# Performance work log

Measured on AMD Instinct MI355X. Metric: run time of the kernel, lower is better.

Reference implementation:

```python
import jax, jax.numpy as jnp
import numpy as np

N, E, B = 50000, 800000, 512
DIN, H, G, M = 128, 128, 32, 128
EPS = 1e-5


def _gcn_layer(h, src, dst, W, b):
    h = h @ W  # [N, H]
    loop = jnp.arange(N)
    s = jnp.concatenate([src, loop])
    d = jnp.concatenate([dst, loop])
    deg = jax.ops.segment_sum(jnp.ones(s.shape, h.dtype), d, num_segments=N)
    dinv = jax.lax.rsqrt(jnp.maximum(deg, 1.0))  # deg >= 1 due to self-loops
    norm = dinv[s] * dinv[d]  # [E+N]
    out = jax.ops.segment_sum(norm[:, None] * h[s], d, num_segments=N)
    return out + b


def _bn_relu(h, gamma, beta):
    mu = jnp.mean(h, axis=0)
    var = jnp.mean((h - mu) ** 2, axis=0)
    return jax.nn.relu((h - mu) * jax.lax.rsqrt(var + EPS) * gamma + beta)


def setup_inputs() -> dict:
    key = jax.random.key(0)
    ks = jax.random.split(key, 20)
    inp = {
        "x": jax.random.normal(ks[0], (N, DIN), jnp.float32),
        "edge_index": jax.random.randint(ks[1], (2, E), 0, N),
        "batch": jnp.sort(jax.random.randint(ks[2], (N,), 0, B)),
        "global_feats": jax.random.normal(ks[3], (B, G), jnp.float32),
    }
    dims = [DIN, H, H]
    for i in range(3):
        inp[f"W{i}"] = jax.random.normal(ks[4 + i], (dims[i], H), jnp.float32) / np.sqrt(dims[i])
        inp[f"b{i}"] = jnp.zeros((H,), jnp.float32)
        inp[f"g{i}"] = jnp.ones((H,), jnp.float32)
        inp[f"be{i}"] = jnp.zeros((H,), jnp.float32)
    inp["M1w"] = jax.random.normal(ks[10], (H + G, M), jnp.float32) / np.sqrt(H + G)
    inp["M1b"] = jnp.zeros((M,), jnp.float32)
    inp["M2w"] = jax.random.normal(ks[11], (M, M // 2), jnp.float32) / np.sqrt(M)
    inp["M2b"] = jnp.zeros((M // 2,), jnp.float32)
    inp["M3w"] = jax.random.normal(ks[12], (M // 2, 1), jnp.float32) / np.sqrt(M // 2)
    inp["M3b"] = jnp.zeros((1,), jnp.float32)
    return inp


def reference(x, edge_index, batch, global_feats,
              W0, b0, g0, be0, W1, b1, g1, be1, W2, b2, g2, be2,
              M1w, M1b, M2w, M2b, M3w, M3b):
    src, dst = edge_index[0], edge_index[1]
    h = x
    for W, b, g, be in ((W0, b0, g0, be0), (W1, b1, g1, be1), (W2, b2, g2, be2)):
        h = _bn_relu(_gcn_layer(h, src, dst, W, b), g, be)
    # global mean pool over graphs
    sums = jax.ops.segment_sum(h, batch, num_segments=B)  # [B, H]
    cnt = jax.ops.segment_sum(jnp.ones((N,), h.dtype), batch, num_segments=B)
    pooled = sums / jnp.maximum(cnt, 1.0)[:, None]
    z = jnp.concatenate([pooled, global_feats], axis=1)  # [B, H+G]
    z = jax.nn.relu(z @ M1w + M1b)
    z = jax.nn.relu(z @ M2w + M2b)
    out = z @ M3w + M3b  # [B, 1]
    return out.reshape(-1)
```

## Files before the change

kernel.cpp:

```cpp
#include <hip/hip_runtime.h>

#define NN 50000
#define NE 800000
#define BG 512
#define HD 128
#define GD 32
#define MD 128
#define EPSV 1e-5f
#define NBK 256
#define BSTR 196
#define BCAP 4096
#define SP 136
#define CSB 128

typedef __attribute__((ext_vector_type(8))) short bf16x8;
typedef __attribute__((ext_vector_type(4))) float f32x4;

static __device__ __forceinline__ unsigned short f2bf(float f) {
    unsigned int u = __float_as_uint(f);
    u += 0x7fffu + ((u >> 16) & 1u);
    return (unsigned short)(u >> 16);
}
static __device__ __forceinline__ float bfu(unsigned short v) {
    return __uint_as_float((unsigned int)v << 16);
}
static __device__ __forceinline__ float bf_lo(unsigned int v) {
    return __uint_as_float(v << 16);
}
static __device__ __forceinline__ float bf_hi(unsigned int v) {
    return __uint_as_float(v & 0xffff0000u);
}

__global__ __launch_bounds__(256) void k_bin(const int* __restrict__ src,
                                             const int* __restrict__ dst,
                                             int* __restrict__ bucket_cnt,
                                             unsigned int* __restrict__ binned) {
    __shared__ int hcnt[NBK];
    __shared__ int hbase[NBK];
    int tid = threadIdx.x;
    int e0 = blockIdx.x * 2048;
    unsigned int pv[8];
    int bk[8], rk[8];
#pragma unroll
    for (int i = 0; i < 8; ++i) {
        int e = e0 + i * 256 + tid;
        if (e < NE) {
            int s = src[e];
            int d = dst[e];
            bk[i] = d / BSTR;
            pv[i] = ((unsigned int)(d - bk[i] * BSTR) << 16) | (unsigned int)s;
        } else {
            bk[i] = -1;
        }
    }
    hcnt[tid] = 0;
    __syncthreads();
#pragma unroll
    for (int i = 0; i < 8; ++i)
        if (bk[i] >= 0) rk[i] = atomicAdd(&hcnt[bk[i]], 1);
    __syncthreads();
    hbase[tid] = atomicAdd(&bucket_cnt[tid], hcnt[tid]);
    __syncthreads();
#pragma unroll
    for (int i = 0; i < 8; ++i)
        if (bk[i] >= 0)
            binned[(size_t)bk[i] * BCAP + hbase[bk[i]] + rk[i]] = pv[i];
}

__global__ __launch_bounds__(256) void k_csr(const unsigned int* __restrict__ binned,
                                             const int* __restrict__ bucket_cnt,
                                             int* __restrict__ offsets,
                                             float* __restrict__ dinv,
                                             int* __restrict__ csr,
                                             const float* __restrict__ W0,
                                             const float* __restrict__ W1,
                                             const float* __restrict__ W2,
                                             unsigned short* __restrict__ Wt) {
    __shared__ unsigned short sW[128 * 130];
    __shared__ int ls[256];
    __shared__ int h[BSTR];
    __shared__ int cur[BSTR];
    __shared__ int bpre_s;
    int b = blockIdx.x, t = threadIdx.x;
    if (b >= NBK) {
        const float* Wsrc = (b == NBK) ? W0 : ((b == NBK + 1) ? W1 : W2);
#pragma unroll
        for (int i = 0; i < 64; ++i) {
            int idx = i * 256 + t;
            int k = idx >> 7, n = idx & 127;
            sW[n * 130 + k] = f2bf(Wsrc[idx]);
        }
        __syncthreads();
        unsigned short* o = Wt + (size_t)(b - NBK) * 16384;
#pragma unroll
        for (int i = 0; i < 64; ++i) {
            int idx = i * 256 + t;
            int n = idx >> 7, k = idx & 127;
            o[idx] = sW[n * 130 + k];
        }
        return;
    }
    int bc = bucket_cnt[t];
    ls[t] = bc;
    __syncthreads();
    for (int off = 1; off < 256; off <<= 1) {
        int c0 = ls[t];
        int add = (t >= off) ? ls[t - off] : 0;
        __syncthreads();
        ls[t] = c0 + add;
        __syncthreads();
    }
    if (t == b) bpre_s = ls[t] - bc;
    if (t < BSTR) h[t] = 0;
    __syncthreads();
    int bpre = bpre_s;
    int nb = bucket_cnt[b];
    const unsigned int* base = binned + (size_t)b * BCAP;
    for (int e = t; e < nb; e += 256)
        atomicAdd(&h[base[e] >> 16], 1);
    __syncthreads();
    int c = (t < BSTR) ? h[t] : 0;
    ls[t] = c;
    __syncthreads();
    for (int off = 1; off < 256; off <<= 1) {
        int c0 = ls[t];
        int add = (t >= off) ? ls[t - off] : 0;
        __syncthreads();
        ls[t] = c0 + add;
        __syncthreads();
    }
    int node = b * BSTR + t;
    if (t < BSTR) {
        int excl = ls[t] - c + bpre;
        cur[t] = excl;
        if (node < NN) {
            offsets[node] = excl;
            dinv[node] = rsqrtf((float)(c + 1));
            if (node == NN - 1) offsets[NN] = NE;
        }
    }
    __syncthreads();
    for (int e = t; e < nb; e += 256) {
        unsigned int v = base[e];
        int pos = atomicAdd(&cur[v >> 16], 1);
        csr[pos] = (int)(v & 0xffffu);
    }
}

__global__ __launch_bounds__(256) void k_gemm(const float* __restrict__ Inf,
                                              const unsigned short* __restrict__ Inh,
                                              const unsigned short* __restrict__ Wt,
                                              unsigned short* __restrict__ Th,
                                              const float* __restrict__ stats,
                                              const float* __restrict__ gamma,
                                              const float* __restrict__ beta,
                                              const float* __restrict__ dinv,
                                              int useBN) {
    __shared__ unsigned short Abf[64 * SP];
    __shared__ unsigned short WtL[128 * SP];
    __shared__ float ssS[256];
    int tid = threadIdx.x;
    int rowBase = blockIdx.x * 64;
    if (useBN) {
        ssS[tid] = stats[tid];
        __syncthreads();
        if (tid < 128) {
            float mu = ssS[tid] * (1.f / NN);
            float var = ssS[128 + tid] * (1.f / NN) - mu * mu;
            float sc = gamma[tid] * rsqrtf(var + EPSV);
            float sh = beta[tid] - mu * sc;
            ssS[tid] = sc;
            ssS[128 + tid] = sh;
        }
        __syncthreads();
#pragma unroll
        for (int i = 0; i < 4; ++i) {
            int q = tid + i * 256;
            int row = q >> 4;
            int k8 = (q & 15) * 8;
            int rg = rowBase + row;
            if (rg >= NN) rg = NN - 1;
            bf16x8 raw = *(const bf16x8*)&Inh[(size_t)rg * HD + k8];
            unsigned short o[8];
#pragma unroll
            for (int e = 0; e < 8; ++e) {
                float v = bfu((unsigned short)raw[e]);
                v = fmaxf(v * ssS[k8 + e] + ssS[128 + k8 + e], 0.f);
                o[e] = f2bf(v);
            }
            *(bf16x8*)&Abf[row * SP + k8] = *(bf16x8*)o;
        }
    } else {
#pragma unroll
        for (int i = 0; i < 8; ++i) {
            int q = tid + i * 256;
            int row = q >> 5;
            int c4 = (q & 31) * 4;
            int rg = rowBase + row;
            if (rg >= NN) rg = NN - 1;
            float4 v = *(const float4*)&Inf[(size_t)rg * HD + c4];
            unsigned short* p = &Abf[row * SP + c4];
            p[0] = f2bf(v.x); p[1] = f2bf(v.y); p[2] = f2bf(v.z); p[3] = f2bf(v.w);
        }
    }
#pragma unroll
    for (int i = 0; i < 8; ++i) {
        int q = tid + i * 256;
        int n = q >> 4;
        int k8 = (q & 15) * 8;
        bf16x8 w = *(const bf16x8*)&Wt[n * HD + k8];
        *(bf16x8*)&WtL[n * SP + k8] = w;
    }
    __syncthreads();
    int lane = tid & 63;
    int wv = tid >> 6;
    int quad = lane >> 4;
    int lrow = wv * 16 + (lane & 15);
    f32x4 acc[8];
#pragma unroll
    for (int c = 0; c < 8; ++c) acc[c] = (f32x4){0.f, 0.f, 0.f, 0.f};
#pragma unroll
    for (int qk = 0; qk < 4; ++qk) {
        int ko = quad * 8 + qk * 32;
        bf16x8 bfr = *(const bf16x8*)&Abf[lrow * SP + ko];
#pragma unroll
        for (int c = 0; c < 8; ++c) {
            bf16x8 afr = *(const bf16x8*)&WtL[(c * 16 + (lane & 15)) * SP + ko];
            acc[c] = __builtin_amdgcn_mfma_f32_16x16x32_bf16(afr, bfr, acc[c], 0, 0, 0);
        }
    }
    int grow = rowBase + lrow;
    if (grow < NN) {
        float di = dinv[grow];
#pragma unroll
        for (int c = 0; c < 8; ++c) {
            ushort4 o;
            o.x = f2bf(acc[c][0] * di);
            o.y = f2bf(acc[c][1] * di);
            o.z = f2bf(acc[c][2] * di);
            o.w = f2bf(acc[c][3] * di);
            *(ushort4*)&Th[(size_t)grow * HD + c * 16 + quad * 4] = o;
        }
    }
}

__global__ __launch_bounds__(256, 8) void k_aggregate(const uint4* __restrict__ T4,
                                                      const int* __restrict__ offsets,
                                                      const int* __restrict__ csr,
                                                      const float* __restrict__ dinv,
                                                      const float* __restrict__ bias,
                                                      unsigned short* __restrict__ Ah) {
    int d = blockIdx.x * 4 + (threadIdx.x >> 6);
    int l = threadIdx.x & 63;
    int half = l >> 4;
    int li = l & 15;
    if (d >= NN) return;
    int start = offsets[d], end = offsets[d + 1];
    float a0 = 0.f, a1 = 0.f, a2 = 0.f, a3 = 0.f;
    float a4 = 0.f, a5 = 0.f, a6 = 0.f, a7 = 0.f;
    int j = start;
    for (; j + 7 < end; j += 8) {
        int s0 = csr[j + half];
        int s1 = csr[j + 4 + half];
        uint4 v0 = T4[(size_t)s0 * 16 + li];
        uint4 v1 = T4[(size_t)s1 * 16 + li];
        a0 += bf_lo(v0.x); a1 += bf_hi(v0.x); a2 += bf_lo(v0.y); a3 += bf_hi(v0.y);
        a4 += bf_lo(v0.z); a5 += bf_hi(v0.z); a6 += bf_lo(v0.w); a7 += bf_hi(v0.w);
        a0 += bf_lo(v1.x); a1 += bf_hi(v1.x); a2 += bf_lo(v1.y); a3 += bf_hi(v1.y);
        a4 += bf_lo(v1.z); a5 += bf_hi(v1.z); a6 += bf_lo(v1.w); a7 += bf_hi(v1.w);
    }
    for (; j + 3 < end; j += 4) {
        int s0 = csr[j + half];
        uint4 v0 = T4[(size_t)s0 * 16 + li];
        a0 += bf_lo(v0.x); a1 += bf_hi(v0.x); a2 += bf_lo(v0.y); a3 += bf_hi(v0.y);
        a4 += bf_lo(v0.z); a5 += bf_hi(v0.z); a6 += bf_lo(v0.w); a7 += bf_hi(v0.w);
    }
    if (j + half < end) {
        int s0 = csr[j + half];
        uint4 v0 = T4[(size_t)s0 * 16 + li];
        a0 += bf_lo(v0.x); a1 += bf_hi(v0.x); a2 += bf_lo(v0.y); a3 += bf_hi(v0.y);
        a4 += bf_lo(v0.z); a5 += bf_hi(v0.z); a6 += bf_lo(v0.w); a7 += bf_hi(v0.w);
    }
    a0 += __shfl_xor(a0, 16); a1 += __shfl_xor(a1, 16);
    a2 += __shfl_xor(a2, 16); a3 += __shfl_xor(a3, 16);
    a4 += __shfl_xor(a4, 16); a5 += __shfl_xor(a5, 16);
    a6 += __shfl_xor(a6, 16); a7 += __shfl_xor(a7, 16);
    a0 += __shfl_xor(a0, 32); a1 += __shfl_xor(a1, 32);
    a2 += __shfl_xor(a2, 32); a3 += __shfl_xor(a3, 32);
    a4 += __shfl_xor(a4, 32); a5 += __shfl_xor(a5, 32);
    a6 += __shfl_xor(a6, 32); a7 += __shfl_xor(a7, 32);
    if (half == 0) {
        float di = dinv[d];
        uint4 vd = T4[(size_t)d * 16 + li];
        float4 bs0 = *(const float4*)&bias[8 * li];
        float4 bs1 = *(const float4*)&bias[8 * li + 4];
        unsigned short o[8];
        o[0] = f2bf(di * (a0 + bf_lo(vd.x)) + bs0.x);
        o[1] = f2bf(di * (a1 + bf_hi(vd.x)) + bs0.y);
        o[2] = f2bf(di * (a2 + bf_lo(vd.y)) + bs0.z);
        o[3] = f2bf(di * (a3 + bf_hi(vd.y)) + bs0.w);
        o[4] = f2bf(di * (a4 + bf_lo(vd.z)) + bs1.x);
        o[5] = f2bf(di * (a5 + bf_hi(vd.z)) + bs1.y);
        o[6] = f2bf(di * (a6 + bf_lo(vd.w)) + bs1.z);
        o[7] = f2bf(di * (a7 + bf_hi(vd.w)) + bs1.w);
        *(bf16x8*)&Ah[(size_t)d * HD + 8 * li] = *(bf16x8*)o;
    }
}

__global__ __launch_bounds__(256) void k_colstats(const uint2* __restrict__ A2,
                                                  float* __restrict__ stats) {
    int li = threadIdx.x & 31;
    int rr = threadIdx.x >> 5;
    float4 s = {0.f, 0.f, 0.f, 0.f}, q = {0.f, 0.f, 0.f, 0.f};
    for (int row = blockIdx.x * 8 + rr; row < NN; row += CSB * 8) {
        uint2 u = A2[(size_t)row * 32 + li];
        float x0 = bf_lo(u.x), x1 = bf_hi(u.x), x2 = bf_lo(u.y), x3 = bf_hi(u.y);
        s.x += x0; s.y += x1; s.z += x2; s.w += x3;
        q.x += x0 * x0; q.y += x1 * x1; q.z += x2 * x2; q.w += x3 * x3;
    }
    __shared__ float4 lsum[256], lqum[256];
    lsum[threadIdx.x] = s;
    lqum[threadIdx.x] = q;
    __syncthreads();
    if (rr == 0) {
        float4 a = lsum[li];
#pragma unroll
        for (int g = 1; g < 8; ++g) {
            float4 b = lsum[g * 32 + li];
            a.x += b.x; a.y += b.y; a.z += b.z; a.w += b.w;
        }
        atomicAdd(&stats[4 * li + 0], a.x);
        atomicAdd(&stats[4 * li + 1], a.y);
        atomicAdd(&stats[4 * li + 2], a.z);
        atomicAdd(&stats[4 * li + 3], a.w);
    } else if (rr == 1) {
        float4 a = lqum[li];
#pragma unroll
        for (int g = 1; g < 8; ++g) {
            float4 b = lqum[g * 32 + li];
            a.x += b.x; a.y += b.y; a.z += b.z; a.w += b.w;
        }
        atomicAdd(&stats[128 + 4 * li + 0], a.x);
        atomicAdd(&stats[128 + 4 * li + 1], a.y);
        atomicAdd(&stats[128 + 4 * li + 2], a.z);
        atomicAdd(&stats[128 + 4 * li + 3], a.w);
    }
}

__global__ __launch_bounds__(256) void k_pool(const unsigned int* __restrict__ Au,
                                              const int* __restrict__ batch,
                                              const float* __restrict__ stats,
                                              const float* __restrict__ gamma,
                                              const float* __restrict__ beta,
                                              float* __restrict__ pooled) {
    __shared__ float ssP[256];
    int t = threadIdx.x;
    ssP[t] = stats[t];
    __syncthreads();
    if (t < 128) {
        float mu = ssP[t] * (1.f / NN);
        float var = ssP[128 + t] * (1.f / NN) - mu * mu;
        float sc = gamma[t] * rsqrtf(var + EPSV);
        float sh = beta[t] - mu * sc;
        ssP[t] = sc;
        ssP[128 + t] = sh;
    }
    __syncthreads();
    int fu = t & 63;
    int half = t >> 6;
    int r0 = blockIdx.x * 64;
    int rend = min(r0 + 64, NN);
    float s0 = ssP[2 * fu], s1 = ssP[2 * fu + 1];
    float h0 = ssP[128 + 2 * fu], h1 = ssP[128 + 2 * fu + 1];
    float a0 = 0.f, a1 = 0.f;
    int cg = -1;
    for (int r = r0 + half; r < rend; r += 4) {
        int g = batch[r];
        if (g != cg) {
            if (cg >= 0) {
                atomicAdd(&pooled[(size_t)cg * HD + 2 * fu], a0);
                atomicAdd(&pooled[(size_t)cg * HD + 2 * fu + 1], a1);
            }
            cg = g;
            a0 = 0.f; a1 = 0.f;
        }
        unsigned int v = Au[(size_t)r * 64 + fu];
        a0 += fmaxf(bf_lo(v) * s0 + h0, 0.f);
        a1 += fmaxf(bf_hi(v) * s1 + h1, 0.f);
    }
    if (cg >= 0) {
        atomicAdd(&pooled[(size_t)cg * HD + 2 * fu], a0);
        atomicAdd(&pooled[(size_t)cg * HD + 2 * fu + 1], a1);
    }
}

__global__ __launch_bounds__(128) void k_mlp(const float* __restrict__ pooled,
                                             const int* __restrict__ batch,
                                             const float* __restrict__ gfeat,
                                             const float* __restrict__ M1w,
                                             const float* __restrict__ M1b,
                                             const float* __restrict__ M2w,
                                             const float* __restrict__ M2b,
                                             const float* __restrict__ M3w,
                                             const float* __restrict__ M3b,
                                             float* __restrict__ out) {
    __shared__ int sb[2];
    __shared__ float z[HD + GD];
    __shared__ float z1[MD];
    __shared__ float z2[MD / 2];
    int b = blockIdx.x, t = threadIdx.x;
    if (t < 2) {
        int val = b + t;
        int lo = 0, hi = NN;
        while (lo < hi) {
            int mid = (lo + hi) >> 1;
            if (batch[mid] < val) lo = mid + 1; else hi = mid;
        }
        sb[t] = lo;
    }
    __syncthreads();
    float ic = 1.f / fmaxf((float)(sb[1] - sb[0]), 1.f);
    z[t] = pooled[(size_t)b * HD + t] * ic;
    if (t < GD) z[HD + t] = gfeat[b * GD + t];
    __syncthreads();
    float a = M1b[t];
    for (int k = 0; k < HD + GD; ++k) a += z[k] * M1w[k * MD + t];
    z1[t] = fmaxf(a, 0.f);
    __syncthreads();
    if (t < MD / 2) {
        float a2 = M2b[t];
        for (int k = 0; k < MD; ++k) a2 += z1[k] * M2w[k * (MD / 2) + t];
        z2[t] = fmaxf(a2, 0.f);
    }
    __syncthreads();
    if (t < 64) {
        float p = z2[t] * M3w[t];
#pragma unroll
        for (int off = 32; off; off >>= 1) p += __shfl_down(p, off);
        if (t == 0) out[b] = p + M3b[0];
    }
}

static inline size_t alg(size_t x) { return (x + 255) & ~(size_t)255; }

extern "C" void kernel_launch(void* const* d_in, const int* in_sizes, int n_in,
                              void* d_out, int out_size, void* d_ws, size_t ws_size,
                              hipStream_t stream) {
    const float* x = (const float*)d_in[0];
    const int* ei = (const int*)d_in[1];
    const int* batch = (const int*)d_in[2];
    const float* gf = (const float*)d_in[3];
    const float* W[3] = {(const float*)d_in[4], (const float*)d_in[8], (const float*)d_in[12]};
    const float* bb[3] = {(const float*)d_in[5], (const float*)d_in[9], (const float*)d_in[13]};
    const float* gg[3] = {(const float*)d_in[6], (const float*)d_in[10], (const float*)d_in[14]};
    const float* be[3] = {(const float*)d_in[7], (const float*)d_in[11], (const float*)d_in[15]};
    const float* M1w = (const float*)d_in[16];
    const float* M1b = (const float*)d_in[17];
    const float* M2w = (const float*)d_in[18];
    const float* M2b = (const float*)d_in[19];
    const float* M3w = (const float*)d_in[20];
    const float* M3b = (const float*)d_in[21];
    float* out = (float*)d_out;

    char* w = (char*)d_ws;
    int* bucket_cnt = (int*)w;    w += alg((size_t)NBK * 4);
    float* pooled = (float*)w;    w += alg((size_t)BG * HD * 4);
    float* stats = (float*)w;     w += alg((size_t)3 * 256 * 4);
    size_t zspan = (size_t)(w - (char*)d_ws);
    int* offsets = (int*)w;       w += alg((size_t)(NN + 1) * 4);
    int* csr = (int*)w;           w += alg((size_t)NE * 4);
    float* dinv = (float*)w;      w += alg((size_t)NN * 4);
    unsigned short* Wt = (unsigned short*)w;  w += alg((size_t)3 * 16384 * 2);
    unsigned int* binned = (unsigned int*)w;  w += alg((size_t)NBK * BCAP * 4);
    unsigned short* Ah = (unsigned short*)w;  w += alg((size_t)NN * HD * 2);
    unsigned short* Th = (unsigned short*)w;  w += alg((size_t)NN * HD * 2);

    const int* src = ei;
    const int* dst = ei + NE;

    hipMemsetAsync(bucket_cnt, 0, zspan, stream);
    k_bin<<<(NE + 2047) / 2048, 256, 0, stream>>>(src, dst, bucket_cnt, binned);
    k_csr<<<NBK + 3, 256, 0, stream>>>(binned, bucket_cnt, offsets, dinv, csr,
                                       W[0], W[1], W[2], Wt);

    for (int L = 0; L < 3; ++L) {
        k_gemm<<<(NN + 63) / 64, 256, 0, stream>>>(x, Ah, Wt + (size_t)L * 16384, Th,
                                                   stats + (L ? (L - 1) * 256 : 0),
                                                   gg[L ? L - 1 : 0], be[L ? L - 1 : 0],
                                                   dinv, L > 0);
        k_aggregate<<<(NN + 3) / 4, 256, 0, stream>>>((const uint4*)Th, offsets, csr,
                                                      dinv, bb[L], Ah);
        k_colstats<<<CSB, 256, 0, stream>>>((const uint2*)Ah, stats + L * 256);
    }

    k_pool<<<(NN + 63) / 64, 256, 0, stream>>>((const unsigned int*)Ah, batch,
                                               stats + 2 * 256, gg[2], be[2], pooled);
    k_mlp<<<BG, 128, 0, stream>>>(pooled, batch, gf, M1w, M1b, M2w, M2b, M3w, M3b, out);
}
```

Measured before the change: 368.4 us.

## Fuse BN column stats into aggregate and pooling into MLP kernel

Column sum and sum-of-squares statistics are now gathered inside k_aggregate through shared-memory atomics, then written to 64 partial slots in global memory that k_gemm and k_mlp add up. This removes the separate k_colstats pass that reread Ah after each layer. k_pool is also dropped: k_mlp now applies BN+ReLU and mean-pools each graph's contiguous node range directly. In exchange every aggregate block does 16 LDS atomics per node and a global atomic per thread, and each MLP block reduces 64 partial slots.

```diff
diff --git a/kernel.cpp b/kernel.cpp
--- a/kernel.cpp
+++ b/kernel.cpp
@@ -11,7 +11,7 @@
 #define BSTR 196
 #define BCAP 4096
 #define SP 136
-#define CSB 128
+#define NSC 64
 
 typedef __attribute__((ext_vector_type(8))) short bf16x8;
 typedef __attribute__((ext_vector_type(4))) float f32x4;
@@ -151,7 +151,7 @@
                                               const unsigned short* __restrict__ Inh,
                                               const unsigned short* __restrict__ Wt,
                                               unsigned short* __restrict__ Th,
-                                              const float* __restrict__ stats,
+                                              const float* __restrict__ statsP,
                                               const float* __restrict__ gamma,
                                               const float* __restrict__ beta,
                                               const float* __restrict__ dinv,
@@ -162,7 +162,9 @@
     int tid = threadIdx.x;
     int rowBase = blockIdx.x * 64;
     if (useBN) {
-        ssS[tid] = stats[tid];
+        float s = 0.f;
+        for (int c = 0; c < NSC; ++c) s += statsP[c * 256 + tid];
+        ssS[tid] = s;
         __syncthreads();
         if (tid < 128) {
             float mu = ssS[tid] * (1.f / NN);
@@ -249,153 +251,88 @@
                                                       const int* __restrict__ csr,
                                                       const float* __restrict__ dinv,
                                                       const float* __restrict__ bias,
-                                                      unsigned short* __restrict__ Ah) {
-    int d = blockIdx.x * 4 + (threadIdx.x >> 6);
-    int l = threadIdx.x & 63;
+                                                      unsigned short* __restrict__ Ah,
+                                                      float* __restrict__ statsP) {
+    __shared__ float sst[256];
+    int tid = threadIdx.x;
+    sst[tid] = 0.f;
+    __syncthreads();
+    int d = blockIdx.x * 4 + (tid >> 6);
+    int l = tid & 63;
     int half = l >> 4;
     int li = l & 15;
-    if (d >= NN) return;
-    int start = offsets[d], end = offsets[d + 1];
-    float a0 = 0.f, a1 = 0.f, a2 = 0.f, a3 = 0.f;
-    float a4 = 0.f, a5 = 0.f, a6 = 0.f, a7 = 0.f;
-    int j = start;
-    for (; j + 7 < end; j += 8) {
-        int s0 = csr[j + half];
-        int s1 = csr[j + 4 + half];
-        uint4 v0 = T4[(size_t)s0 * 16 + li];
-        uint4 v1 = T4[(size_t)s1 * 16 + li];
-        a0 += bf_lo(v0.x); a1 += bf_hi(v0.x); a2 += bf_lo(v0.y); a3 += bf_hi(v0.y);
-        a4 += bf_lo(v0.z); a5 += bf_hi(v0.z); a6 += bf_lo(v0.w); a7 += bf_hi(v0.w);
-        a0 += bf_lo(v1.x); a1 += bf_hi(v1.x); a2 += bf_lo(v1.y); a3 += bf_hi(v1.y);
-        a4 += bf_lo(v1.z); a5 += bf_hi(v1.z); a6 += bf_lo(v1.w); a7 += bf_hi(v1.w);
-    }
-    for (; j + 3 < end; j += 4) {
-        int s0 = csr[j + half];
-        uint4 v0 = T4[(size_t)s0 * 16 + li];
-        a0 += bf_lo(v0.x); a1 += bf_hi(v0.x); a2 += bf_lo(v0.y); a3 += bf_hi(v0.y);
-        a4 += bf_lo(v0.z); a5 += bf_hi(v0.z); a6 += bf_lo(v0.w); a7 += bf_hi(v0.w);
-    }
-    if (j + half < end) {
-        int s0 = csr[j + half];
-        uint4 v0 = T4[(size_t)s0 * 16 + li];
-        a0 += bf_lo(v0.x); a1 += bf_hi(v0.x); a2 += bf_lo(v0.y); a3 += bf_hi(v0.y);
-        a4 += bf_lo(v0.z); a5 += bf_hi(v0.z); a6 += bf_lo(v0.w); a7 += bf_hi(v0.w);
-    }
-    a0 += __shfl_xor(a0, 16); a1 += __shfl_xor(a1, 16);
-    a2 += __shfl_xor(a2, 16); a3 += __shfl_xor(a3, 16);
-    a4 += __shfl_xor(a4, 16); a5 += __shfl_xor(a5, 16);
-    a6 += __shfl_xor(a6, 16); a7 += __shfl_xor(a7, 16);
-    a0 += __shfl_xor(a0, 32); a1 += __shfl_xor(a1, 32);
-    a2 += __shfl_xor(a2, 32); a3 += __shfl_xor(a3, 32);
-    a4 += __shfl_xor(a4, 32); a5 += __shfl_xor(a5, 32);
-    a6 += __shfl_xor(a6, 32); a7 += __shfl_xor(a7, 32);
-    if (half == 0) {
-        float di = dinv[d];
-        uint4 vd = T4[(size_t)d * 16 + li];
-        float4 bs0 = *(const float4*)&bias[8 * li];
-        float4 bs1 = *(const float4*)&bias[8 * li + 4];
-        unsigned short o[8];
-        o[0] = f2bf(di * (a0 + bf_lo(vd.x)) + bs0.x);
-        o[1] = f2bf(di * (a1 + bf_hi(vd.x)) + bs0.y);
-        o[2] = f2bf(di * (a2 + bf_lo(vd.y)) + bs0.z);
-        o[3] = f2bf(di * (a3 + bf_hi(vd.y)) + bs0.w);
-        o[4] = f2bf(di * (a4 + bf_lo(vd.z)) + bs1.x);
-        o[5] = f2bf(di * (a5 + bf_hi(vd.z)) + bs1.y);
-        o[6] = f2bf(di * (a6 + bf_lo(vd.w)) + bs1.z);
-        o[7] = f2bf(di * (a7 + bf_hi(vd.w)) + bs1.w);
-        *(bf16x8*)&Ah[(size_t)d * HD + 8 * li] = *(bf16x8*)o;
-    }
-}
-
-__global__ __launch_bounds__(256) void k_colstats(const uint2* __restrict__ A2,
-                                                  float* __restrict__ stats) {
-    int li = threadIdx.x & 31;
-    int rr = threadIdx.x >> 5;
-    float4 s = {0.f, 0.f, 0.f, 0.f}, q = {0.f, 0.f, 0.f, 0.f};
-    for (int row = blockIdx.x * 8 + rr; row < NN; row += CSB * 8) {
-        uint2 u = A2[(size_t)row * 32 + li];
-        float x0 = bf_lo(u.x), x1 = bf_hi(u.x), x2 = bf_lo(u.y), x3 = bf_hi(u.y);
-        s.x += x0; s.y += x1; s.z += x2; s.w += x3;
-        q.x += x0 * x0; q.y += x1 * x1; q.z += x2 * x2; q.w += x3 * x3;
-    }
-    __shared__ float4 lsum[256], lqum[256];
-    lsum[threadIdx.x] = s;
-    lqum[threadIdx.x] = q;
-    __syncthreads();
-    if (rr == 0) {
-        float4 a = lsum[li];
-#pragma unroll
-        for (int g = 1; g < 8; ++g) {
-            float4 b = lsum[g * 32 + li];
-            a.x += b.x; a.y += b.y; a.z += b.z; a.w += b.w;
-        }
-        atomicAdd(&stats[4 * li + 0], a.x);
-        atomicAdd(&stats[4 * li + 1], a.y);
-        atomicAdd(&stats[4 * li + 2], a.z);
-        atomicAdd(&stats[4 * li + 3], a.w);
-    } else if (rr == 1) {
-        float4 a = lqum[li];
-#pragma unroll
-        for (int g = 1; g < 8; ++g) {
-            float4 b = lqum[g * 32 + li];
-            a.x += b.x; a.y += b.y; a.z += b.z; a.w += b.w;
-        }
-        atomicAdd(&stats[128 + 4 * li + 0], a.x);
-        atomicAdd(&stats[128 + 4 * li + 1], a.y);
-        atomicAdd(&stats[128 + 4 * li + 2], a.z);
-        atomicAdd(&stats[128 + 4 * li + 3], a.w);
-    }
-}
-
-__global__ __launch_bounds__(256) void k_pool(const unsigned int* __restrict__ Au,
-                                              const int* __restrict__ batch,
-                                              const float* __restrict__ stats,
-                                              const float* __restrict__ gamma,
-                                              const float* __restrict__ beta,
-                                              float* __restrict__ pooled) {
-    __shared__ float ssP[256];
-    int t = threadIdx.x;
-    ssP[t] = stats[t];
-    __syncthreads();
-    if (t < 128) {
-        float mu = ssP[t] * (1.f / NN);
-        float var = ssP[128 + t] * (1.f / NN) - mu * mu;
-        float sc = gamma[t] * rsqrtf(var + EPSV);
-        float sh = beta[t] - mu * sc;
-        ssP[t] = sc;
-        ssP[128 + t] = sh;
-    }
-    __syncthreads();
-    int fu = t & 63;
-    int half = t >> 6;
-    int r0 = blockIdx.x * 64;
-    int rend = min(r0 + 64, NN);
-    float s0 = ssP[2 * fu], s1 = ssP[2 * fu + 1];
-    float h0 = ssP[128 + 2 * fu], h1 = ssP[128 + 2 * fu + 1];
-    float a0 = 0.f, a1 = 0.f;
-    int cg = -1;
-    for (int r = r0 + half; r < rend; r += 4) {
-        int g = batch[r];
-        if (g != cg) {
-            if (cg >= 0) {
-                atomicAdd(&pooled[(size_t)cg * HD + 2 * fu], a0);
-                atomicAdd(&pooled[(size_t)cg * HD + 2 * fu + 1], a1);
-            }
-            cg = g;
-            a0 = 0.f; a1 = 0.f;
-        }
-        unsigned int v = Au[(size_t)r * 64 + fu];
-        a0 += fmaxf(bf_lo(v) * s0 + h0, 0.f);
-        a1 += fmaxf(bf_hi(v) * s1 + h1, 0.f);
-    }
-    if (cg >= 0) {
-        atomicAdd(&pooled[(size_t)cg * HD + 2 * fu], a0);
-        atomicAdd(&pooled[(size_t)cg * HD + 2 * fu + 1], a1);
-    }
-}
-
-__global__ __launch_bounds__(128) void k_mlp(const float* __restrict__ pooled,
+    if (d < NN) {
+        int start = offsets[d], end = offsets[d + 1];
+        float a0 = 0.f, a1 = 0.f, a2 = 0.f, a3 = 0.f;
+        float a4 = 0.f, a5 = 0.f, a6 = 0.f, a7 = 0.f;
+        int j = start;
+        for (; j + 7 < end; j += 8) {
+            int s0 = csr[j + half];
+            int s1 = csr[j + 4 + half];
+            uint4 v0 = T4[(size_t)s0 * 16 + li];
+            uint4 v1 = T4[(size_t)s1 * 16 + li];
+            a0 += bf_lo(v0.x); a1 += bf_hi(v0.x); a2 += bf_lo(v0.y); a3 += bf_hi(v0.y);
+            a4 += bf_lo(v0.z); a5 += bf_hi(v0.z); a6 += bf_lo(v0.w); a7 += bf_hi(v0.w);
+            a0 += bf_lo(v1.x); a1 += bf_hi(v1.x); a2 += bf_lo(v1.y); a3 += bf_hi(v1.y);
+            a4 += bf_lo(v1.z); a5 += bf_hi(v1.z); a6 += bf_lo(v1.w); a7 += bf_hi(v1.w);
+        }
+        for (; j + 3 < end; j += 4) {
+            int s0 = csr[j + half];
+            uint4 v0 = T4[(size_t)s0 * 16 + li];
+            a0 += bf_lo(v0.x); a1 += bf_hi(v0.x); a2 += bf_lo(v0.y); a3 += bf_hi(v0.y);
+            a4 += bf_lo(v0.z); a5 += bf_hi(v0.z); a6 += bf_lo(v0.w); a7 += bf_hi(v0.w);
+        }
+        if (j + half < end) {
+            int s0 = csr[j + half];
+            uint4 v0 = T4[(size_t)s0 * 16 + li];
+            a0 += bf_lo(v0.x); a1 += bf_hi(v0.x); a2 += bf_lo(v0.y); a3 += bf_hi(v0.y);
+            a4 += bf_lo(v0.z); a5 += bf_hi(v0.z); a6 += bf_lo(v0.w); a7 += bf_hi(v0.w);
+        }
+        a0 += __shfl_xor(a0, 16); a1 += __shfl_xor(a1, 16);
+        a2 += __shfl_xor(a2, 16); a3 += __shfl_xor(a3, 16);
+        a4 += __shfl_xor(a4, 16); a5 += __shfl_xor(a5, 16);
+        a6 += __shfl_xor(a6, 16); a7 += __shfl_xor(a7, 16);
+        a0 += __shfl_xor(a0, 32); a1 += __shfl_xor(a1, 32);
+        a2 += __shfl_xor(a2, 32); a3 += __shfl_xor(a3, 32);
+        a4 += __shfl_xor(a4, 32); a5 += __shfl_xor(a5, 32);
+        a6 += __shfl_xor(a6, 32); a7 += __shfl_xor(a7, 32);
+        if (half == 0) {
+            float di = dinv[d];
+            uint4 vd = T4[(size_t)d * 16 + li];
+            float4 bs0 = *(const float4*)&bias[8 * li];
+            float4 bs1 = *(const float4*)&bias[8 * li + 4];
+            float v0 = di * (a0 + bf_lo(vd.x)) + bs0.x;
+            float v1 = di * (a1 + bf_hi(vd.x)) + bs0.y;
+            float v2 = di * (a2 + bf_lo(vd.y)) + bs0.z;
+            float v3 = di * (a3 + bf_hi(vd.y)) + bs0.w;
+            float v4 = di * (a4 + bf_lo(vd.z)) + bs1.x;
+            float v5 = di * (a5 + bf_hi(vd.z)) + bs1.y;
+            float v6 = di * (a6 + bf_lo(vd.w)) + bs1.z;
+            float v7 = di * (a7 + bf_hi(vd.w)) + bs1.w;
+            int fb = 8 * li;
+            atomicAdd(&sst[fb + 0], v0); atomicAdd(&sst[fb + 1], v1);
+            atomicAdd(&sst[fb + 2], v2); atomicAdd(&sst[fb + 3], v3);
+            atomicAdd(&sst[fb + 4], v4); atomicAdd(&sst[fb + 5], v5);
+            atomicAdd(&sst[fb + 6], v6); atomicAdd(&sst[fb + 7], v7);
+            atomicAdd(&sst[128 + fb + 0], v0 * v0); atomicAdd(&sst[128 + fb + 1], v1 * v1);
+            atomicAdd(&sst[128 + fb + 2], v2 * v2); atomicAdd(&sst[128 + fb + 3], v3 * v3);
+            atomicAdd(&sst[128 + fb + 4], v4 * v4); atomicAdd(&sst[128 + fb + 5], v5 * v5);
+            atomicAdd(&sst[128 + fb + 6], v6 * v6); atomicAdd(&sst[128 + fb + 7], v7 * v7);
+            unsigned short o[8];
+            o[0] = f2bf(v0); o[1] = f2bf(v1); o[2] = f2bf(v2); o[3] = f2bf(v3);
+            o[4] = f2bf(v4); o[5] = f2bf(v5); o[6] = f2bf(v6); o[7] = f2bf(v7);
+            *(bf16x8*)&Ah[(size_t)d * HD + 8 * li] = *(bf16x8*)o;
+        }
+    }
+    __syncthreads();
+    atomicAdd(&statsP[(blockIdx.x & (NSC - 1)) * 256 + tid], sst[tid]);
+}
+
+__global__ __launch_bounds__(128) void k_mlp(const unsigned short* __restrict__ Ah,
                                              const int* __restrict__ batch,
+                                             const float* __restrict__ statsP,
+                                             const float* __restrict__ gamma,
+                                             const float* __restrict__ beta,
                                              const float* __restrict__ gfeat,
                                              const float* __restrict__ M1w,
                                              const float* __restrict__ M1b,
@@ -405,6 +342,8 @@
                                              const float* __restrict__ M3b,
                                              float* __restrict__ out) {
     __shared__ int sb[2];
+    __shared__ float ssc[128], ssh[128];
+    __shared__ float zp[4][128];
     __shared__ float z[HD + GD];
     __shared__ float z1[MD];
     __shared__ float z2[MD / 2];
@@ -418,9 +357,39 @@
         }
         sb[t] = lo;
     }
-    __syncthreads();
-    float ic = 1.f / fmaxf((float)(sb[1] - sb[0]), 1.f);
-    z[t] = pooled[(size_t)b * HD + t] * ic;
+    float s = 0.f, q = 0.f;
+    for (int c = 0; c < NSC; ++c) {
+        s += statsP[c * 256 + t];
+        q += statsP[c * 256 + 128 + t];
+    }
+    {
+        float mu = s * (1.f / NN);
+        float var = q * (1.f / NN) - mu * mu;
+        float sc = gamma[t] * rsqrtf(var + EPSV);
+        ssc[t] = sc;
+        ssh[t] = beta[t] - mu * sc;
+    }
+    __syncthreads();
+    int s0 = sb[0], s1 = sb[1];
+    int grp = t >> 5, u = t & 31;
+    float c0 = ssc[4 * u], c1 = ssc[4 * u + 1], c2 = ssc[4 * u + 2], c3 = ssc[4 * u + 3];
+    float h0 = ssh[4 * u], h1 = ssh[4 * u + 1], h2 = ssh[4 * u + 2], h3 = ssh[4 * u + 3];
+    float p0 = 0.f, p1 = 0.f, p2 = 0.f, p3 = 0.f;
+    const uint2* A2 = (const uint2*)Ah;
+    for (int r = s0 + grp; r < s1; r += 4) {
+        uint2 v = A2[(size_t)r * 32 + u];
+        p0 += fmaxf(bf_lo(v.x) * c0 + h0, 0.f);
+        p1 += fmaxf(bf_hi(v.x) * c1 + h1, 0.f);
+        p2 += fmaxf(bf_lo(v.y) * c2 + h2, 0.f);
+        p3 += fmaxf(bf_hi(v.y) * c3 + h3, 0.f);
+    }
+    zp[grp][4 * u + 0] = p0;
+    zp[grp][4 * u + 1] = p1;
+    zp[grp][4 * u + 2] = p2;
+    zp[grp][4 * u + 3] = p3;
+    __syncthreads();
+    float ic = 1.f / fmaxf((float)(s1 - s0), 1.f);
+    z[t] = (zp[0][t] + zp[1][t] + zp[2][t] + zp[3][t]) * ic;
     if (t < GD) z[HD + t] = gfeat[b * GD + t];
     __syncthreads();
     float a = M1b[t];
@@ -464,8 +433,7 @@
 
     char* w = (char*)d_ws;
     int* bucket_cnt = (int*)w;    w += alg((size_t)NBK * 4);
-    float* pooled = (float*)w;    w += alg((size_t)BG * HD * 4);
-    float* stats = (float*)w;     w += alg((size_t)3 * 256 * 4);
+    float* statsP = (float*)w;    w += alg((size_t)3 * NSC * 256 * 4);
     size_t zspan = (size_t)(w - (char*)d_ws);
     int* offsets = (int*)w;       w += alg((size_t)(NN + 1) * 4);
     int* csr = (int*)w;           w += alg((size_t)NE * 4);
@@ -485,15 +453,14 @@
 
     for (int L = 0; L < 3; ++L) {
         k_gemm<<<(NN + 63) / 64, 256, 0, stream>>>(x, Ah, Wt + (size_t)L * 16384, Th,
-                                                   stats + (L ? (L - 1) * 256 : 0),
+                                                   statsP + (L ? (L - 1) * NSC * 256 : 0),
                                                    gg[L ? L - 1 : 0], be[L ? L - 1 : 0],
                                                    dinv, L > 0);
         k_aggregate<<<(NN + 3) / 4, 256, 0, stream>>>((const uint4*)Th, offsets, csr,
-                                                      dinv, bb[L], Ah);
-        k_colstats<<<CSB, 256, 0, stream>>>((const uint2*)Ah, stats + L * 256);
-    }
-
-    k_pool<<<(NN + 63) / 64, 256, 0, stream>>>((const unsigned int*)Ah, batch,
-                                               stats + 2 * 256, gg[2], be[2], pooled);
-    k_mlp<<<BG, 128, 0, stream>>>(pooled, batch, gf, M1w, M1b, M2w, M2b, M3w, M3b, out);
-}
+                                                      dinv, bb[L], Ah,
+                                                      statsP + (size_t)L * NSC * 256);
+    }
+
+    k_mlp<<<BG, 128, 0, stream>>>(Ah, batch, statsP + (size_t)2 * NSC * 256,
+                                  gg[2], be[2], gf, M1w, M1b, M2w, M2b, M3w, M3b, out);
+}
```

Result: slower. 463.5 us (+25.8%).
